# Kernel optimization log

Measured on AMD Instinct MI355X. Metric: run time of the kernel, lower is better.

Reference implementation:

```python
import jax, jax.numpy as jnp
import numpy as np

B, L, H = 4, 512, 768          # batch, seq_len, bert hidden
S, R = 100, 100                # num candidate spans, num relation pairs
E = 128                        # size embedding dim
TE, TR = 8, 6                  # entity / relation types
MAX_ENT_LEN = 100
NEG = -1e20


def _span_masks(rng, b, n, seq_len, max_len):
    # contiguous span masks with lengths in [1, max_len-1] so sum(-1) < max_len
    starts = rng.integers(0, seq_len - 1, size=(b, n))
    lengths = rng.integers(1, max_len, size=(b, n))
    ends = np.minimum(starts + lengths, seq_len)
    pos = np.arange(seq_len)
    m = (pos[None, None, :] >= starts[..., None]) & (pos[None, None, :] < ends[..., None])
    return jnp.asarray(m.astype(np.int32))


def setup_inputs() -> dict:
    rng = np.random.default_rng(0)
    key = jax.random.key(0)
    k = jax.random.split(key, 6)
    return {
        "last_hidden_state": jax.random.normal(k[0], (B, L, H), jnp.float32),
        "entity_mask": _span_masks(rng, B, S, L, MAX_ENT_LEN),
        "relations": jnp.asarray(rng.integers(0, S, size=(B, R, 2)).astype(np.int32)),
        "relation_context_mask": _span_masks(rng, B, R, L, MAX_ENT_LEN),
        "relation_sample_mask": jnp.asarray(rng.integers(0, 2, size=(B, R)).astype(np.int32)),
        "size_emb": jax.random.normal(k[1], (MAX_ENT_LEN, E), jnp.float32) * 0.02,
        "span_w": jax.random.normal(k[2], (E + 2 * H, TE), jnp.float32) * 0.02,
        "span_b": jnp.zeros((TE,), jnp.float32),
        "rel_w": jax.random.normal(k[3], (2 * E + 3 * H, TR), jnp.float32) * 0.02,
        "rel_b": jnp.zeros((TR,), jnp.float32),
    }


def _masked_max(h, mask):
    # h: [B,L,H], mask: [B,N,L] int {0,1} -> [B,N,H]
    mf = mask[..., None].astype(h.dtype)                       # [B,N,L,1]
    masked = jnp.where(mf == 0, jnp.asarray(NEG, h.dtype), h[:, None] * mf)
    return masked.max(axis=2)


def reference(last_hidden_state, entity_mask, relations, relation_context_mask,
              relation_sample_mask, size_emb, span_w, span_b, rel_w, rel_b):
    b = last_hidden_state.shape[0]
    # ---- entity classification ----
    context = last_hidden_state[:, 0]                          # CLS pooling [B,H]
    entity_size = size_emb[entity_mask.sum(-1)]                # [B,S,E]
    entity = _masked_max(last_hidden_state, entity_mask)       # [B,S,H]
    ctx = jnp.broadcast_to(context[:, None], (b, entity.shape[1], context.shape[-1]))
    entity_repr = jnp.concatenate([entity, ctx, entity_size], axis=-1)
    entity_logit = entity_repr @ span_w + span_b               # [B,S,TE]
    # ---- relation classification ----
    rel_ctx = _masked_max(last_hidden_state, relation_context_mask)  # [B,R,H]
    rel_ctx = jnp.where(relation_sample_mask[..., None] == 1,
                        jnp.zeros((), rel_ctx.dtype), rel_ctx)
    r = relations.shape[1]
    flat = relations.reshape(b, r * 2)                         # [B,2R]
    pair = jnp.take_along_axis(entity, flat[..., None], axis=1).reshape(b, r, -1)      # [B,R,2H]
    pair_size = jnp.take_along_axis(entity_size, flat[..., None], axis=1).reshape(b, r, -1)  # [B,R,2E]
    relation_repr = jnp.concatenate([rel_ctx, pair, pair_size], axis=-1)
    relation_logit = relation_repr @ rel_w + rel_b             # [B,R,TR]
    return entity_logit, relation_logit
```

## Files before the change

### kernel.cpp

```cpp
#include <hip/hip_runtime.h>

#define Bn 4
#define Ln 512
#define Hn 768
#define Sn 100
#define Rn 100
#define En 128
#define TEn 8
#define TRn 6
#define NEGF (-1e20f)
#define H4 (Hn / 4)
#define E4 (En / 4)
#define NTHR 640
#define WBLK 16
#define NJ (Ln / WBLK)
#define DCH 64
#define NDCH (H4 / DCH)

__device__ __forceinline__ float4 fmax4(float4 a, float4 b) {
    return make_float4(fmaxf(a.x, b.x), fmaxf(a.y, b.y),
                       fmaxf(a.z, b.z), fmaxf(a.w, b.w));
}

__global__ void __launch_bounds__(64)
win16_kernel(const float* __restrict__ hid, float* __restrict__ win) {
    int blk = blockIdx.x;
    int c = blk % NDCH;
    int t = blk / NDCH;
    int j = t % NJ, b = t / NJ;
    int d4 = c * DCH + threadIdx.x;
    int base = j * WBLK;

    const float4* hb4 = (const float4*)(hid + (size_t)b * Ln * Hn) + d4;
    float4 row[WBLK];
    #pragma unroll
    for (int k = 0; k < WBLK; ++k)
        row[k] = hb4[(size_t)(base + k) * H4];
    #pragma unroll
    for (int k = WBLK - 2; k >= 0; --k)
        row[k] = fmax4(row[k], row[k + 1]);

    float4* w4 = (float4*)(win + ((size_t)b * Ln + base) * Hn) + d4;
    w4[0] = row[0];
    bool has_next = (j < NJ - 1);
    float4 pre = has_next ? hb4[(size_t)(base + WBLK) * H4]
                          : make_float4(NEGF, NEGF, NEGF, NEGF);
    #pragma unroll
    for (int k = 1; k < WBLK; ++k) {
        w4[(size_t)k * H4] = fmax4(row[k], pre);
        if (k < WBLK - 1 && has_next)
            pre = fmax4(pre, hb4[(size_t)(base + WBLK + k) * H4]);
    }
}

__device__ __forceinline__ void scan_span(const int* __restrict__ mask,
                                          int lane, int* start, int* end) {
    const int4* m4 = (const int4*)(mask + lane * 8);
    int4 a = m4[0], c = m4[1];
    int mm[8] = {a.x, a.y, a.z, a.w, c.x, c.y, c.z, c.w};
    int first = 0x7fffffff, last = -1;
    #pragma unroll
    for (int r = 0; r < 8; ++r) {
        if (mm[r] != 0) {
            int row = lane * 8 + r;
            first = min(first, row);
            last = max(last, row);
        }
    }
    #pragma unroll
    for (int off = 1; off < 64; off <<= 1) {
        first = min(first, __shfl_xor(first, off, 64));
        last = max(last, __shfl_xor(last, off, 64));
    }
    *start = first;
    *end = last + 1;
}

__device__ __forceinline__ float4 wmax(const float4* __restrict__ hb4,
                                       const float4* __restrict__ wn4,
                                       int s, int e) {
    float4 m0 = make_float4(NEGF, NEGF, NEGF, NEGF);
    float4 m1 = m0;
    int cnt = e - s;
    if (cnt >= WBLK) {
        int r = s;
        for (; r + 2 * WBLK <= e; r += 2 * WBLK) {
            m0 = fmax4(m0, wn4[(size_t)r * H4]);
            m1 = fmax4(m1, wn4[(size_t)(r + WBLK) * H4]);
        }
        if (r + WBLK <= e) { m0 = fmax4(m0, wn4[(size_t)r * H4]); r += WBLK; }
        if (r < e) m1 = fmax4(m1, wn4[(size_t)(e - WBLK) * H4]);
    } else {
        int r = s;
        for (; r + 2 <= e; r += 2) {
            m0 = fmax4(m0, hb4[(size_t)r * H4]);
            m1 = fmax4(m1, hb4[(size_t)(r + 1) * H4]);
        }
        if (r < e) m0 = fmax4(m0, hb4[(size_t)r * H4]);
    }
    return fmax4(m0, m1);
}

__global__ void __launch_bounds__(NTHR)
logits_kernel(const float* __restrict__ hid,
              const int* __restrict__ ent_mask,
              const int* __restrict__ rel_mask,
              const int* __restrict__ samp_mask,
              const int* __restrict__ relations,
              const float* __restrict__ size_emb,
              const float* __restrict__ span_w,
              const float* __restrict__ span_b,
              const float* __restrict__ rel_w,
              const float* __restrict__ rel_b,
              const float* __restrict__ win,
              float* __restrict__ out_ent,
              float* __restrict__ out_rel) {
    int blk = blockIdx.x;
    int tid = threadIdx.x;
    int lane = tid & 63, wv = tid >> 6;

    __shared__ int se[3][2];
    __shared__ float red[10][TEn];

    float acc[TEn];
    #pragma unroll
    for (int t = 0; t < TEn; ++t) acc[t] = 0.0f;

    if (blk < Bn * Sn) {
        int b = blk / Sn;
        float w32[4 * TEn];
        if (tid < 384 + E4) {
            const float4* wp = (const float4*)(span_w + (size_t)tid * 4 * TEn);
            float4* wreg = (float4*)w32;
            #pragma unroll
            for (int i = 0; i < TEn; ++i) wreg[i] = wp[i];
        }
        if (wv == 0) {
            int s0, e0;
            scan_span(ent_mask + (size_t)blk * Ln, lane, &s0, &e0);
            if (lane == 0) { se[0][0] = s0; se[0][1] = e0; }
        }
        __syncthreads();
        int start = se[0][0], end = se[0][1];
        int cnt = end - start;

        const float4* hb4 = (const float4*)(hid + (size_t)b * Ln * Hn);
        const float4* wn4 = (const float4*)(win + (size_t)b * Ln * Hn);
        float4 v = make_float4(0.f, 0.f, 0.f, 0.f);
        bool active = true;
        if (tid < 192) {
            v = wmax(hb4 + tid, wn4 + tid, start, end);
        } else if (tid < 384) {
            v = hb4[tid - 192];
        } else if (tid < 384 + E4) {
            v = ((const float4*)(size_emb + (size_t)cnt * En))[tid - 384];
        } else {
            active = false;
        }
        if (active) {
            const float* vp = &v.x;
            #pragma unroll
            for (int j = 0; j < 4; ++j)
                #pragma unroll
                for (int t = 0; t < TEn; ++t)
                    acc[t] += vp[j] * w32[j * TEn + t];
        }

        #pragma unroll
        for (int t = 0; t < TEn; ++t)
            #pragma unroll
            for (int off = 32; off > 0; off >>= 1)
                acc[t] += __shfl_down(acc[t], off, 64);
        if (lane == 0) {
            #pragma unroll
            for (int t = 0; t < TEn; ++t) red[wv][t] = acc[t];
        }
        __syncthreads();
        if (tid < TEn) {
            float s = span_b[tid];
            #pragma unroll
            for (int w = 0; w < 10; ++w) s += red[w][tid];
            out_ent[(size_t)blk * TEn + tid] = s;
        }
    } else {
        int rblk = blk - Bn * Sn;
        int b = rblk / Rn;
        int a0 = relations[rblk * 2 + 0];
        int a1 = relations[rblk * 2 + 1];
        bool samp = (samp_mask[rblk] == 1);

        float w24[4 * TRn];
        {
            const float4* wp = (const float4*)(rel_w + (size_t)tid * 4 * TRn);
            float4* wreg = (float4*)w24;
            #pragma unroll
            for (int i = 0; i < TRn; ++i) wreg[i] = wp[i];
        }

        if (wv == 0) {
            if (!samp) {
                int s0, e0;
                scan_span(rel_mask + (size_t)rblk * Ln, lane, &s0, &e0);
                if (lane == 0) { se[0][0] = s0; se[0][1] = e0; }
            }
        } else if (wv == 1) {
            int s1, e1;
            scan_span(ent_mask + ((size_t)b * Sn + a0) * Ln, lane, &s1, &e1);
            if (lane == 0) { se[1][0] = s1; se[1][1] = e1; }
        } else if (wv == 2) {
            int s2, e2;
            scan_span(ent_mask + ((size_t)b * Sn + a1) * Ln, lane, &s2, &e2);
            if (lane == 0) { se[2][0] = s2; se[2][1] = e2; }
        }
        __syncthreads();
        int cnt0 = se[1][1] - se[1][0];
        int cnt1 = se[2][1] - se[2][0];

        const float4* hb4 = (const float4*)(hid + (size_t)b * Ln * Hn);
        const float4* wn4 = (const float4*)(win + (size_t)b * Ln * Hn);
        float4 v = make_float4(0.f, 0.f, 0.f, 0.f);
        bool active = true;
        if (tid < 192) {
            if (samp) active = false;
            else v = wmax(hb4 + tid, wn4 + tid, se[0][0], se[0][1]);
        } else if (tid < 384) {
            int u = tid - 192;
            v = wmax(hb4 + u, wn4 + u, se[1][0], se[1][1]);
        } else if (tid < 576) {
            int u = tid - 384;
            v = wmax(hb4 + u, wn4 + u, se[2][0], se[2][1]);
        } else if (tid < 576 + E4) {
            v = ((const float4*)(size_emb + (size_t)cnt0 * En))[tid - 576];
        } else {
            v = ((const float4*)(size_emb + (size_t)cnt1 * En))[tid - 576 - E4];
        }
        if (active) {
            const float* vp = &v.x;
            #pragma unroll
            for (int j = 0; j < 4; ++j)
                #pragma unroll
                for (int t = 0; t < TRn; ++t)
                    acc[t] += vp[j] * w24[j * TRn + t];
        }

        #pragma unroll
        for (int t = 0; t < TRn; ++t)
            #pragma unroll
            for (int off = 32; off > 0; off >>= 1)
                acc[t] += __shfl_down(acc[t], off, 64);
        if (lane == 0) {
            #pragma unroll
            for (int t = 0; t < TRn; ++t) red[wv][t] = acc[t];
        }
        __syncthreads();
        if (tid < TRn) {
            float s = rel_b[tid];
            #pragma unroll
            for (int w = 0; w < 10; ++w) s += red[w][tid];
            out_rel[(size_t)rblk * TRn + tid] = s;
        }
    }
}

extern "C" void kernel_launch(void* const* d_in, const int* in_sizes, int n_in,
                              void* d_out, int out_size, void* d_ws, size_t ws_size,
                              hipStream_t stream) {
    const float* hid       = (const float*)d_in[0];
    const int*   ent_mask  = (const int*)d_in[1];
    const int*   relations = (const int*)d_in[2];
    const int*   rel_mask  = (const int*)d_in[3];
    const int*   samp_mask = (const int*)d_in[4];
    const float* size_emb  = (const float*)d_in[5];
    const float* span_w    = (const float*)d_in[6];
    const float* span_b    = (const float*)d_in[7];
    const float* rel_w     = (const float*)d_in[8];
    const float* rel_b     = (const float*)d_in[9];

    float* out = (float*)d_out;
    float* out_ent = out;
    float* out_rel = out + Bn * Sn * TEn;

    float* win = (float*)d_ws;

    win16_kernel<<<Bn * NJ * NDCH, 64, 0, stream>>>(hid, win);

    logits_kernel<<<Bn * (Sn + Rn), NTHR, 0, stream>>>(
        hid, ent_mask, rel_mask, samp_mask, relations, size_emb,
        span_w, span_b, rel_w, rel_b, win, out_ent, out_rel);
}
```

Measured before the change: 23.81 us.

## Drop windowed-max precompute kernel and scan spans directly from hidden states

Removes the separate kernel that built 16-row suffix/prefix window maxima in workspace, and computes span maxima by streaming every row of the span directly from the hidden state with a 4-way unrolled loop. This eliminates one launch and a full write of a hidden-sized buffer. In exchange, each span now loads all of its rows instead of a few window lookups, raising cache traffic and per-thread serial load count.

```diff
diff --git a/kernel.cpp b/kernel.cpp
--- a/kernel.cpp
+++ b/kernel.cpp
@@ -12,45 +12,10 @@
 #define H4 (Hn / 4)
 #define E4 (En / 4)
 #define NTHR 640
-#define WBLK 16
-#define NJ (Ln / WBLK)
-#define DCH 64
-#define NDCH (H4 / DCH)
 
 __device__ __forceinline__ float4 fmax4(float4 a, float4 b) {
     return make_float4(fmaxf(a.x, b.x), fmaxf(a.y, b.y),
                        fmaxf(a.z, b.z), fmaxf(a.w, b.w));
-}
-
-__global__ void __launch_bounds__(64)
-win16_kernel(const float* __restrict__ hid, float* __restrict__ win) {
-    int blk = blockIdx.x;
-    int c = blk % NDCH;
-    int t = blk / NDCH;
-    int j = t % NJ, b = t / NJ;
-    int d4 = c * DCH + threadIdx.x;
-    int base = j * WBLK;
-
-    const float4* hb4 = (const float4*)(hid + (size_t)b * Ln * Hn) + d4;
-    float4 row[WBLK];
-    #pragma unroll
-    for (int k = 0; k < WBLK; ++k)
-        row[k] = hb4[(size_t)(base + k) * H4];
-    #pragma unroll
-    for (int k = WBLK - 2; k >= 0; --k)
-        row[k] = fmax4(row[k], row[k + 1]);
-
-    float4* w4 = (float4*)(win + ((size_t)b * Ln + base) * Hn) + d4;
-    w4[0] = row[0];
-    bool has_next = (j < NJ - 1);
-    float4 pre = has_next ? hb4[(size_t)(base + WBLK) * H4]
-                          : make_float4(NEGF, NEGF, NEGF, NEGF);
-    #pragma unroll
-    for (int k = 1; k < WBLK; ++k) {
-        w4[(size_t)k * H4] = fmax4(row[k], pre);
-        if (k < WBLK - 1 && has_next)
-            pre = fmax4(pre, hb4[(size_t)(base + WBLK + k) * H4]);
-    }
 }
 
 __device__ __forceinline__ void scan_span(const int* __restrict__ mask,
@@ -76,45 +41,35 @@
     *end = last + 1;
 }
 
-__device__ __forceinline__ float4 wmax(const float4* __restrict__ hb4,
-                                       const float4* __restrict__ wn4,
-                                       int s, int e) {
+__device__ __forceinline__ float4 stream_max(const float4* __restrict__ hb4,
+                                             int s, int e) {
     float4 m0 = make_float4(NEGF, NEGF, NEGF, NEGF);
-    float4 m1 = m0;
-    int cnt = e - s;
-    if (cnt >= WBLK) {
-        int r = s;
-        for (; r + 2 * WBLK <= e; r += 2 * WBLK) {
-            m0 = fmax4(m0, wn4[(size_t)r * H4]);
-            m1 = fmax4(m1, wn4[(size_t)(r + WBLK) * H4]);
-        }
-        if (r + WBLK <= e) { m0 = fmax4(m0, wn4[(size_t)r * H4]); r += WBLK; }
-        if (r < e) m1 = fmax4(m1, wn4[(size_t)(e - WBLK) * H4]);
-    } else {
-        int r = s;
-        for (; r + 2 <= e; r += 2) {
-            m0 = fmax4(m0, hb4[(size_t)r * H4]);
-            m1 = fmax4(m1, hb4[(size_t)(r + 1) * H4]);
-        }
-        if (r < e) m0 = fmax4(m0, hb4[(size_t)r * H4]);
-    }
-    return fmax4(m0, m1);
+    float4 m1 = m0, m2 = m0, m3 = m0;
+    int r = s;
+    for (; r + 4 <= e; r += 4) {
+        m0 = fmax4(m0, hb4[(size_t)(r + 0) * H4]);
+        m1 = fmax4(m1, hb4[(size_t)(r + 1) * H4]);
+        m2 = fmax4(m2, hb4[(size_t)(r + 2) * H4]);
+        m3 = fmax4(m3, hb4[(size_t)(r + 3) * H4]);
+    }
+    for (; r < e; ++r)
+        m0 = fmax4(m0, hb4[(size_t)r * H4]);
+    return fmax4(fmax4(m0, m1), fmax4(m2, m3));
 }
 
 __global__ void __launch_bounds__(NTHR)
-logits_kernel(const float* __restrict__ hid,
-              const int* __restrict__ ent_mask,
-              const int* __restrict__ rel_mask,
-              const int* __restrict__ samp_mask,
-              const int* __restrict__ relations,
-              const float* __restrict__ size_emb,
-              const float* __restrict__ span_w,
-              const float* __restrict__ span_b,
-              const float* __restrict__ rel_w,
-              const float* __restrict__ rel_b,
-              const float* __restrict__ win,
-              float* __restrict__ out_ent,
-              float* __restrict__ out_rel) {
+fused_kernel(const float* __restrict__ hid,
+             const int* __restrict__ ent_mask,
+             const int* __restrict__ rel_mask,
+             const int* __restrict__ samp_mask,
+             const int* __restrict__ relations,
+             const float* __restrict__ size_emb,
+             const float* __restrict__ span_w,
+             const float* __restrict__ span_b,
+             const float* __restrict__ rel_w,
+             const float* __restrict__ rel_b,
+             float* __restrict__ out_ent,
+             float* __restrict__ out_rel) {
     int blk = blockIdx.x;
     int tid = threadIdx.x;
     int lane = tid & 63, wv = tid >> 6;
@@ -145,11 +100,10 @@
         int cnt = end - start;
 
         const float4* hb4 = (const float4*)(hid + (size_t)b * Ln * Hn);
-        const float4* wn4 = (const float4*)(win + (size_t)b * Ln * Hn);
         float4 v = make_float4(0.f, 0.f, 0.f, 0.f);
         bool active = true;
         if (tid < 192) {
-            v = wmax(hb4 + tid, wn4 + tid, start, end);
+            v = stream_max(hb4 + tid, start, end);
         } else if (tid < 384) {
             v = hb4[tid - 192];
         } else if (tid < 384 + E4) {
@@ -217,18 +171,17 @@
         int cnt1 = se[2][1] - se[2][0];
 
         const float4* hb4 = (const float4*)(hid + (size_t)b * Ln * Hn);
-        const float4* wn4 = (const float4*)(win + (size_t)b * Ln * Hn);
         float4 v = make_float4(0.f, 0.f, 0.f, 0.f);
         bool active = true;
         if (tid < 192) {
             if (samp) active = false;
-            else v = wmax(hb4 + tid, wn4 + tid, se[0][0], se[0][1]);
+            else v = stream_max(hb4 + tid, se[0][0], se[0][1]);
         } else if (tid < 384) {
             int u = tid - 192;
-            v = wmax(hb4 + u, wn4 + u, se[1][0], se[1][1]);
+            v = stream_max(hb4 + u, se[1][0], se[1][1]);
         } else if (tid < 576) {
             int u = tid - 384;
-            v = wmax(hb4 + u, wn4 + u, se[2][0], se[2][1]);
+            v = stream_max(hb4 + u, se[2][0], se[2][1]);
         } else if (tid < 576 + E4) {
             v = ((const float4*)(size_emb + (size_t)cnt0 * En))[tid - 576];
         } else {
@@ -280,11 +233,7 @@
     float* out_ent = out;
     float* out_rel = out + Bn * Sn * TEn;
 
-    float* win = (float*)d_ws;
-
-    win16_kernel<<<Bn * NJ * NDCH, 64, 0, stream>>>(hid, win);
-
-    logits_kernel<<<Bn * (Sn + Rn), NTHR, 0, stream>>>(
+    fused_kernel<<<Bn * (Sn + Rn), NTHR, 0, stream>>>(
         hid, ent_mask, rel_mask, samp_mask, relations, size_emb,
-        span_w, span_b, rel_w, rel_b, win, out_ent, out_rel);
-}
+        span_w, span_b, rel_w, rel_b, out_ent, out_rel);
+}
```

New measurement: 29.43 us. 23.6% more time.
